# Performance work log

Measured on AMD Instinct MI355X. Metric: run time of the kernel, lower is better.

Reference implementation:

```python
import jax, jax.numpy as jnp
import numpy as np

B = 2048          # env batch
N = 32            # num_svgd_particles
D = 6             # act_dim
OBS = 17          # obs_dim
H = 256           # q1 hidden width
STEPS = 10        # num_svgd_steps
LR = 0.1          # svgd_lr
LIMIT = 1.0       # act_limit
LOG_NP1 = np.float32(np.log(N + 1.0))


def setup_inputs() -> dict:
    key = jax.random.key(0)
    ks = jax.random.split(key, 6)
    obs = jax.random.normal(ks[0], (B * N, OBS), dtype=jnp.float32)
    a = jax.random.normal(ks[1], (B * N, D), dtype=jnp.float32)
    W1 = jax.random.normal(ks[2], (OBS + D, H), dtype=jnp.float32) / np.float32(np.sqrt(OBS + D))
    b1 = jnp.zeros((H,), dtype=jnp.float32)
    W2 = jax.random.normal(ks[3], (H, H), dtype=jnp.float32) / np.float32(np.sqrt(H))
    b2 = jnp.zeros((H,), dtype=jnp.float32)
    W3 = jax.random.normal(ks[4], (H, 1), dtype=jnp.float32) / np.float32(np.sqrt(H))
    b3 = jnp.zeros((1,), dtype=jnp.float32)
    return {"obs": obs, "a": a, "W1": W1, "b1": b1, "W2": W2, "b2": b2, "W3": W3, "b3": b3}


def q1(obs, X, W1, b1, W2, b2, W3, b3):
    # standard SAC critic: Q(s, a) = MLP(concat(s, a))
    h = jax.nn.relu(jnp.concatenate([obs, X], axis=-1) @ W1 + b1)
    h = jax.nn.relu(h @ W2 + b2)
    return (h @ W3 + b3).squeeze(-1)


def rbf(X):
    # X: (B, N, D); input_2 = X.detach() in the original
    Xd = jax.lax.stop_gradient(X)
    diff = X[:, :, None, :] - Xd[:, None, :, :]          # (B, N, N, D)
    dist_sq = jnp.sum(diff * diff, axis=-1)              # (B, N, N)
    nn = N * N
    # torch.median returns the LOWER of the two middle values for even counts
    med = jnp.sort(jax.lax.stop_gradient(dist_sq).reshape(-1, nn), axis=1)[:, (nn - 1) // 2]
    h = med / (2.0 * LOG_NP1)                            # bandwidth^2 (sigma^2 = h)
    gamma = 1.0 / (1e-8 + 2.0 * h)                       # (B,)
    gamma = gamma[:, None, None]                         # (B, 1, 1)
    kappa = jnp.exp(-gamma * dist_sq)                    # (B, N, N)
    kappa_grad = -2.0 * (diff * gamma[..., None]) * kappa[..., None]  # (B, N, N, D)
    return kappa, diff, gamma, kappa_grad


def reference(obs, a, W1, b1, W2, b2, W3, b3):
    score_fn = jax.grad(lambda Xf: q1(obs, Xf, W1, b1, W2, b2, W3, b3).sum())
    logp = jnp.zeros((B, N), dtype=jnp.float32)

    for _ in range(STEPS):
        score = score_fn(a)                              # (B*N, D)
        X = a.reshape(B, N, D)
        s = score.reshape(B, N, D)
        K_XX, K_diff, K_gamma, K_grad = rbf(X)
        Kd = jax.lax.stop_gradient(K_XX)
        phi = (jnp.einsum('bij,bjd->bid', Kd, s) - K_grad.sum(axis=2)) / N  # (B, N, D)
        line_4 = (K_grad * s[:, None, :, :]).sum(-1).mean(-1)               # (B, N)
        line_5 = -2.0 * K_gamma[:, :, 0] * (
            (-K_grad * K_diff).sum(-1) - D * K_XX
        ).mean(-1)                                                          # (B, N)
        logp = logp - LR * (line_4 + line_5)
        a = jnp.clip(a + LR * phi.reshape(B * N, D), -LIMIT, LIMIT)
        a = jax.lax.stop_gradient(a)

    return a, logp
```

## Files before the change

### kernel.cpp

```cpp
#include <hip/hip_runtime.h>
#include <hip/hip_bf16.h>

#define NB 2048
#define NP 32
#define ND 6
#define NOBS 17
#define NH 256
#define NSTEPS 10
#define C_LR 0.1f
#define C_LIM 1.0f
#define C_LOGNP1 3.4965075614664802f

typedef __bf16 bf16x8 __attribute__((ext_vector_type(8)));
typedef float  f32x4  __attribute__((ext_vector_type(4)));

#define MFMA(a, b, c) __builtin_amdgcn_mfma_f32_16x16x32_bf16(a, b, c, 0, 0, 0)

static __device__ __forceinline__ unsigned short f2bf(float f) {
    union { float f; unsigned u; } c; c.f = f;
    const unsigned r = c.u + 0x7fffu + ((c.u >> 16) & 1u);
    return (unsigned short)(r >> 16);
}

static __device__ __forceinline__ int colpf(int n) {
    return ((n >> 5) << 11) + (((n >> 3) & 3) << 7) + (n & 7);
}

__global__ void prep_swizzle(const float* __restrict__ W1, const float* __restrict__ W2,
                             unsigned short* __restrict__ ws) {
    const int g = blockIdx.x * 256 + threadIdx.x;
    unsigned short v[8];
    if (g < 8192) {
        const int l = g & 63, fid = g >> 6;
        const int kt = fid >> 4, nt = fid & 15;
        const int row0 = kt * 32 + (l >> 4) * 8;
        const int col  = nt * 16 + (l & 15);
#pragma unroll
        for (int j = 0; j < 8; ++j) v[j] = f2bf(W2[(row0 + j) * NH + col]);
        ushort4* dst = (ushort4*)(ws + (size_t)g * 8);
        dst[0] = make_ushort4(v[0], v[1], v[2], v[3]);
        dst[1] = make_ushort4(v[4], v[5], v[6], v[7]);
    } else if (g < 16384) {
        const int e = g - 8192;
        const int l = e & 63, fid = e >> 6;
        const int kt = fid >> 4, nt = fid & 15;
        const int row  = nt * 16 + (l & 15);
        const int col0 = kt * 32 + (l >> 4) * 8;
#pragma unroll
        for (int j = 0; j < 8; ++j) v[j] = f2bf(W2[row * NH + col0 + j]);
        ushort4* dst = (ushort4*)(ws + 65536 + (size_t)e * 8);
        dst[0] = make_ushort4(v[0], v[1], v[2], v[3]);
        dst[1] = make_ushort4(v[4], v[5], v[6], v[7]);
    } else if (g < 16896) {
        const int e = g - 16384;
        const int l = e & 63, kt = e >> 6;
        const int n  = l & 15;
        const int k0 = kt * 32 + (l >> 4) * 8;
#pragma unroll
        for (int j = 0; j < 8; ++j)
            v[j] = (n < ND) ? f2bf(W1[(NOBS + n) * NH + k0 + j]) : (unsigned short)0;
        ushort4* dst = (ushort4*)(ws + 131072 + (size_t)e * 8);
        dst[0] = make_ushort4(v[0], v[1], v[2], v[3]);
        dst[1] = make_ushort4(v[4], v[5], v[6], v[7]);
    } else if (g < 17920) {
        const int e = g - 16896;
        const int l = e & 63, nt = e >> 6;
        const int col = nt * 16 + (l & 15);
        const int r0  = (l >> 4) * 8;
#pragma unroll
        for (int j = 0; j < 8; ++j)
            v[j] = (r0 + j < NOBS + ND) ? f2bf(W1[(r0 + j) * NH + col]) : (unsigned short)0;
        ushort4* dst = (ushort4*)(ws + 135168 + (size_t)e * 8);
        dst[0] = make_ushort4(v[0], v[1], v[2], v[3]);
        dst[1] = make_ushort4(v[4], v[5], v[6], v[7]);
    }
}

__global__ __launch_bounds__(256, 4)
void svgd_kernel(const float* __restrict__ obs, const float* __restrict__ a_in,
                 const float* __restrict__ W1, const float* __restrict__ b1,
                 const float* __restrict__ W2, const float* __restrict__ b2,
                 const float* __restrict__ W3, const unsigned short* __restrict__ ws,
                 float* __restrict__ out)
{
    __shared__ __attribute__((aligned(16))) unsigned short hA[64 * NH];
    __shared__ float Xs[2][384];
    __shared__ float sc_[512];
    __shared__ float med_s[2];

    const int t    = threadIdx.x;
    const int bb   = blockIdx.x;
    const int lane = t & 63;
    const int wid  = t >> 6;
    const int w4   = wid * 4;
    const int quad = lane >> 4;
    const int ln15 = lane & 15;
    const int qo = t >> 7, iao = (t & 127) >> 2, jgo = t & 3;

    const unsigned short* gW2f = ws;
    const unsigned short* gW2b = ws + 65536;
    const unsigned short* gW1p = ws + 131072;
    const unsigned short* gW1f = ws + 135168;

    {
        float* scr = (float*)hA;
        const float* obs_g = obs + (size_t)bb * 1088;
        for (int p = t; p < 1088; p += 256) scr[p] = obs_g[p];
        const float* a_g = a_in + (size_t)bb * 384;
        for (int p = t; p < 384; p += 256) Xs[0][p] = a_g[p];
    }
    __syncthreads();
    bf16x8 a0[4];
    {
        const float* scr = (const float*)hA;
#pragma unroll
        for (int m = 0; m < 4; ++m) {
            const int s = m * 16 + ln15;
#pragma unroll
            for (int j = 0; j < 8; ++j) {
                const int k = quad * 8 + j;
                float v = 0.0f;
                if (k < NOBS) v = scr[s * NOBS + k];
                else if (k < NOBS + ND) v = Xs[0][s * 6 + (k - NOBS)];
                a0[m][j] = (__bf16)v;
            }
        }
    }
    __syncthreads();

    float b1r[4], b2r[4]; unsigned short w3u[4];
#pragma unroll
    for (int q = 0; q < 4; ++q) {
        const int n = (w4 + q) * 16 + ln15;
        b1r[q] = b1[n]; b2r[q] = b2[n]; w3u[q] = f2bf(W3[n]);
    }

    float logp_r = 0.0f;
    int cur = 0;
    const f32x4 zv = {0.f, 0.f, 0.f, 0.f};

    for (int step = 0; step < NSTEPS; ++step) {
        unsigned long long mask1 = 0ull;
        {
            bf16x8 w1B[4];
#pragma unroll
            for (int q = 0; q < 4; ++q)
                w1B[q] = *(const bf16x8*)(gW1f + ((w4 + q) * 64 + lane) * 8);
            f32x4 acc0[4][4];
#pragma unroll
            for (int m = 0; m < 4; ++m)
#pragma unroll
                for (int q = 0; q < 4; ++q) acc0[m][q] = MFMA(a0[m], w1B[q], zv);
#pragma unroll
            for (int q = 0; q < 4; ++q) {
                const int cp = colpf((w4 + q) * 16 + ln15);
#pragma unroll
                for (int m = 0; m < 4; ++m)
#pragma unroll
                    for (int reg = 0; reg < 4; ++reg) {
                        const float hv = acc0[m][q][reg] + b1r[q];
                        const int idx = cp + m * 512 + (quad * 4 + reg) * 8;
                        if (hv > 0.f) {
                            mask1 |= 1ull << (q * 16 + m * 4 + reg);
                            hA[idx] = f2bf(hv);
                        } else hA[idx] = 0;
                    }
            }
        }
        __syncthreads();

        {
            f32x4 acc[4][4];
#pragma unroll
            for (int m = 0; m < 4; ++m)
#pragma unroll
                for (int q = 0; q < 4; ++q) acc[m][q] = zv;
#pragma unroll 2
            for (int kt = 0; kt < 8; ++kt) {
                bf16x8 a[4];
#pragma unroll
                for (int m = 0; m < 4; ++m)
                    a[m] = *(const bf16x8*)&hA[(kt * 4 + m) * 512 + lane * 8];
#pragma unroll
                for (int q = 0; q < 4; ++q) {
                    const bf16x8 bf = *(const bf16x8*)(gW2f + ((kt * 16 + w4 + q) * 64 + lane) * 8);
#pragma unroll
                    for (int m = 0; m < 4; ++m) acc[m][q] = MFMA(a[m], bf, acc[m][q]);
                }
            }
            __syncthreads();
#pragma unroll
            for (int q = 0; q < 4; ++q) {
                const int cp = colpf((w4 + q) * 16 + ln15);
                const float b2v = b2r[q];
                const unsigned short w3v = w3u[q];
#pragma unroll
                for (int m = 0; m < 4; ++m)
#pragma unroll
                    for (int reg = 0; reg < 4; ++reg) {
                        const int idx = cp + m * 512 + (quad * 4 + reg) * 8;
                        hA[idx] = (acc[m][q][reg] + b2v > 0.f) ? w3v : (unsigned short)0;
                    }
            }
        }
        __syncthreads();

        {
            f32x4 acc2[4][4];
#pragma unroll
            for (int m = 0; m < 4; ++m)
#pragma unroll
                for (int q = 0; q < 4; ++q) acc2[m][q] = zv;
#pragma unroll 2
            for (int kt = 0; kt < 8; ++kt) {
                bf16x8 a[4];
#pragma unroll
                for (int m = 0; m < 4; ++m)
                    a[m] = *(const bf16x8*)&hA[(kt * 4 + m) * 512 + lane * 8];
#pragma unroll
                for (int q = 0; q < 4; ++q) {
                    const bf16x8 bf = *(const bf16x8*)(gW2b + ((kt * 16 + w4 + q) * 64 + lane) * 8);
#pragma unroll
                    for (int m = 0; m < 4; ++m) acc2[m][q] = MFMA(a[m], bf, acc2[m][q]);
                }
            }
            __syncthreads();
#pragma unroll
            for (int q = 0; q < 4; ++q) {
                const int cp = colpf((w4 + q) * 16 + ln15);
#pragma unroll
                for (int m = 0; m < 4; ++m)
#pragma unroll
                    for (int reg = 0; reg < 4; ++reg) {
                        const int idx = cp + m * 512 + (quad * 4 + reg) * 8;
                        hA[idx] = ((mask1 >> (q * 16 + m * 4 + reg)) & 1ull)
                                      ? f2bf(acc2[m][q][reg]) : (unsigned short)0;
                    }
            }
        }
        __syncthreads();

        if (wid >= 2) {
            const int mb = (wid - 2) * 2;
            f32x4 sa[2] = {zv, zv};
#pragma unroll
            for (int kt = 0; kt < 8; ++kt) {
                const bf16x8 bw = *(const bf16x8*)(gW1p + (kt * 64 + lane) * 8);
#pragma unroll
                for (int mm = 0; mm < 2; ++mm) {
                    const bf16x8 a = *(const bf16x8*)&hA[(kt * 4 + mb + mm) * 512 + lane * 8];
                    sa[mm] = MFMA(a, bw, sa[mm]);
                }
            }
            if (ln15 < ND) {
#pragma unroll
                for (int mm = 0; mm < 2; ++mm)
#pragma unroll
                    for (int reg = 0; reg < 4; ++reg)
                        sc_[((mb + mm) * 16 + quad * 4 + reg) * 8 + ln15] = sa[mm][reg];
            }
        } else {
            const float* Xc = &Xs[cur][wid * 192];
            unsigned u[8];
#pragma unroll
            for (int r = 0; r < 8; ++r) {
                const int e = lane + 64 * r;
                if (e < 496) {
                    int i = (int)((63.0f - sqrtf(3969.0f - 8.0f * (float)e)) * 0.5f);
                    while (i * (63 - i) / 2 > e) --i;
                    while ((i + 1) * (62 - i) / 2 <= e) ++i;
                    const int j = i + 1 + (e - i * (63 - i) / 2);
                    float s = 0.f;
#pragma unroll
                    for (int d = 0; d < ND; ++d) {
                        const float df = Xc[i * 6 + d] - Xc[j * 6 + d];
                        s += df * df;
                    }
                    u[r] = __float_as_uint(s);
                } else u[r] = 0x7f800000u;
            }
            unsigned P = 0u;
            for (int bit = 30; bit >= 0; --bit) {
                const unsigned Q = P | (1u << bit);
                int c = 0;
#pragma unroll
                for (int r = 0; r < 8; ++r)
                    c += __popcll(__ballot(u[r] < Q));
                if (c <= 239) P = Q;
            }
            if (lane == 0) med_s[wid] = __uint_as_float(P);
        }
        __syncthreads();

        {
            const int nxt = cur ^ 1;
            const float gam = 1.0f / (1e-8f + med_s[qo] / C_LOGNP1);
            const float* Xc = &Xs[cur][qo * 192];
            float xi[6];
#pragma unroll
            for (int d = 0; d < ND; ++d) xi[d] = Xc[iao * 6 + d];
            float w[8] = {0, 0, 0, 0, 0, 0, 0, 0};
#pragma unroll
            for (int jj = 0; jj < 8; ++jj) {
                const int j = jgo * 8 + jj;
                float df6[6], sj6[6];
                float dsv = 0.f, dot = 0.f;
#pragma unroll
                for (int d = 0; d < ND; ++d) {
                    df6[d] = xi[d] - Xc[j * 6 + d];
                    sj6[d] = sc_[(qo * 32 + j) * 8 + d];
                    dsv += df6[d] * df6[d];
                    dot += df6[d] * sj6[d];
                }
                const float kap = __expf(-gam * dsv);
                const float tg = 2.0f * gam * kap;
#pragma unroll
                for (int d = 0; d < ND; ++d) w[d] += kap * sj6[d] + tg * df6[d];
                w[6] -= tg * dot;
                w[7] += tg * dsv - 6.0f * kap;
            }
#pragma unroll
            for (int off = 1; off < 4; off <<= 1)
#pragma unroll
                for (int c = 0; c < 8; ++c) w[c] += __shfl_xor(w[c], off);
            const int base = (qo * 32 + iao) * 6;
            {
                float x = xi[jgo] + C_LR * (w[jgo] * (1.0f / 32.0f));
                Xs[nxt][base + jgo] = fminf(fmaxf(x, -C_LIM), C_LIM);
            }
            if (jgo < 2) {
                const int d = jgo + 4;
                float x = xi[d] + C_LR * (w[d] * (1.0f / 32.0f));
                Xs[nxt][base + d] = fminf(fmaxf(x, -C_LIM), C_LIM);
            }
            if (jgo == 3)
                logp_r -= C_LR * (w[6] * (1.0f / 32.0f)
                                  - 2.0f * gam * (w[7] * (1.0f / 32.0f)));
        }
        __syncthreads();

        cur ^= 1;
        if (quad == 2) {
#pragma unroll
            for (int m = 0; m < 4; ++m) {
                const int s = m * 16 + ln15;
#pragma unroll
                for (int j = 1; j <= 6; ++j)
                    a0[m][j] = (__bf16)Xs[cur][s * 6 + (j - 1)];
            }
        }
    }

    for (int p = t; p < 384; p += 256) out[(size_t)bb * 384 + p] = Xs[cur][p];
    if (jgo == 3) out[(size_t)NB * NP * ND + bb * 64 + qo * 32 + iao] = logp_r;
}

extern "C" void kernel_launch(void* const* d_in, const int* in_sizes, int n_in,
                              void* d_out, int out_size, void* d_ws, size_t ws_size,
                              hipStream_t stream) {
    const float* obs = (const float*)d_in[0];
    const float* a   = (const float*)d_in[1];
    const float* W1  = (const float*)d_in[2];
    const float* b1  = (const float*)d_in[3];
    const float* W2  = (const float*)d_in[4];
    const float* b2  = (const float*)d_in[5];
    const float* W3  = (const float*)d_in[6];
    unsigned short* wsu = (unsigned short*)d_ws;
    float* out = (float*)d_out;

    prep_swizzle<<<70, 256, 0, stream>>>(W1, W2, wsu);
    svgd_kernel<<<NB / 2, 256, 0, stream>>>(obs, a, W1, b1, W2, b2, W3, wsu, out);
}
```

Baseline: 488.4 us.

## Swizzle LDS layouts, pack bf16 conversions, vectorize particle loads, shorten median search

The hidden-activation buffer hA is written and read through an XOR-swizzled address pattern to cut LDS bank conflicts in the MFMA operand loads. ReLU outputs are now converted two at a time with v_cvt_pk_bf16_f32 instead of the manual rounding helper. Particle positions and scores are padded to a stride of 8 floats with a swizzle, so each particle is read with one 4-wide and one 2-wide vector load. The median bisection stops at bit 8, which saves ballot iterations but leaves the low mantissa bits of the median at zero, a small approximation in the bandwidth.

```diff
diff --git a/kernel.cpp b/kernel.cpp
--- a/kernel.cpp
+++ b/kernel.cpp
@@ -13,6 +13,7 @@
 
 typedef __bf16 bf16x8 __attribute__((ext_vector_type(8)));
 typedef float  f32x4  __attribute__((ext_vector_type(4)));
+typedef float  f32x2  __attribute__((ext_vector_type(2)));
 
 #define MFMA(a, b, c) __builtin_amdgcn_mfma_f32_16x16x32_bf16(a, b, c, 0, 0, 0)
 
@@ -22,9 +23,17 @@
     return (unsigned short)(r >> 16);
 }
 
+static __device__ __forceinline__ unsigned cvtpk_bf16(float lo, float hi) {
+    unsigned r;
+    asm("v_cvt_pk_bf16_f32 %0, %1, %2" : "=v"(r) : "v"(lo), "v"(hi));
+    return r;
+}
+
 static __device__ __forceinline__ int colpf(int n) {
     return ((n >> 5) << 11) + (((n >> 3) & 3) << 7) + (n & 7);
 }
+
+#define XSW(p) ((((p) >> 3) & 3) << 3)
 
 __global__ void prep_swizzle(const float* __restrict__ W1, const float* __restrict__ W2,
                              unsigned short* __restrict__ ws) {
@@ -84,8 +93,8 @@
                  float* __restrict__ out)
 {
     __shared__ __attribute__((aligned(16))) unsigned short hA[64 * NH];
-    __shared__ float Xs[2][384];
-    __shared__ float sc_[512];
+    __shared__ __attribute__((aligned(16))) float Xs[2][512];
+    __shared__ __attribute__((aligned(16))) float sc_[512];
     __shared__ float med_s[2];
 
     const int t    = threadIdx.x;
@@ -97,6 +106,11 @@
     const int ln15 = lane & 15;
     const int qo = t >> 7, iao = (t & 127) >> 2, jgo = t & 3;
 
+    const int lb = (((lane >> 2) & 3) << 3)
+                 | (((lane & 3) ^ ((lane >> 4) & 1)) << 5)
+                 | ((lane >> 4) << 7);
+    const int x5t = ((ln15 >> 3) & 1) << 5;
+
     const unsigned short* gW2f = ws;
     const unsigned short* gW2b = ws + 65536;
     const unsigned short* gW1p = ws + 131072;
@@ -107,7 +121,10 @@
         const float* obs_g = obs + (size_t)bb * 1088;
         for (int p = t; p < 1088; p += 256) scr[p] = obs_g[p];
         const float* a_g = a_in + (size_t)bb * 384;
-        for (int p = t; p < 384; p += 256) Xs[0][p] = a_g[p];
+        for (int e = t; e < 384; e += 256) {
+            const int p = e / 6, d = e - p * 6;
+            Xs[0][((p * 8) ^ XSW(p)) + d] = a_g[e];
+        }
     }
     __syncthreads();
     bf16x8 a0[4];
@@ -121,7 +138,7 @@
                 const int k = quad * 8 + j;
                 float v = 0.0f;
                 if (k < NOBS) v = scr[s * NOBS + k];
-                else if (k < NOBS + ND) v = Xs[0][s * 6 + (k - NOBS)];
+                else if (k < NOBS + ND) v = Xs[0][((s * 8) ^ XSW(s)) + (k - NOBS)];
                 a0[m][j] = (__bf16)v;
             }
         }
@@ -153,18 +170,29 @@
                 for (int q = 0; q < 4; ++q) acc0[m][q] = MFMA(a0[m], w1B[q], zv);
 #pragma unroll
             for (int q = 0; q < 4; ++q) {
-                const int cp = colpf((w4 + q) * 16 + ln15);
-#pragma unroll
-                for (int m = 0; m < 4; ++m)
-#pragma unroll
-                    for (int reg = 0; reg < 4; ++reg) {
-                        const float hv = acc0[m][q][reg] + b1r[q];
-                        const int idx = cp + m * 512 + (quad * 4 + reg) * 8;
-                        if (hv > 0.f) {
-                            mask1 |= 1ull << (q * 16 + m * 4 + reg);
-                            hA[idx] = f2bf(hv);
-                        } else hA[idx] = 0;
-                    }
+                const int cq = colpf((w4 + q) * 16 + ln15) + quad * 8;
+                const int ax0 = (cq     ) ^ x5t;
+                const int ax1 = (cq + 32) ^ x5t;
+                const int ax2 = (cq + 64) ^ x5t;
+                const int ax3 = (cq + 96) ^ x5t;
+                const float b1v = b1r[q];
+#pragma unroll
+                for (int m = 0; m < 4; ++m) {
+                    const float f0 = acc0[m][q][0] + b1v;
+                    const float f1 = acc0[m][q][1] + b1v;
+                    const float f2 = acc0[m][q][2] + b1v;
+                    const float f3 = acc0[m][q][3] + b1v;
+                    if (f0 > 0.f) mask1 |= 1ull << (q * 16 + m * 4 + 0);
+                    if (f1 > 0.f) mask1 |= 1ull << (q * 16 + m * 4 + 1);
+                    if (f2 > 0.f) mask1 |= 1ull << (q * 16 + m * 4 + 2);
+                    if (f3 > 0.f) mask1 |= 1ull << (q * 16 + m * 4 + 3);
+                    const unsigned pk01 = cvtpk_bf16(fmaxf(f0, 0.f), fmaxf(f1, 0.f));
+                    const unsigned pk23 = cvtpk_bf16(fmaxf(f2, 0.f), fmaxf(f3, 0.f));
+                    hA[ax0 + m * 512] = (unsigned short)pk01;
+                    hA[ax1 + m * 512] = (unsigned short)(pk01 >> 16);
+                    hA[ax2 + m * 512] = (unsigned short)pk23;
+                    hA[ax3 + m * 512] = (unsigned short)(pk23 >> 16);
+                }
             }
         }
         __syncthreads();
@@ -180,7 +208,7 @@
                 bf16x8 a[4];
 #pragma unroll
                 for (int m = 0; m < 4; ++m)
-                    a[m] = *(const bf16x8*)&hA[(kt * 4 + m) * 512 + lane * 8];
+                    a[m] = *(const bf16x8*)&hA[(kt * 4 + m) * 512 + lb];
 #pragma unroll
                 for (int q = 0; q < 4; ++q) {
                     const bf16x8 bf = *(const bf16x8*)(gW2f + ((kt * 16 + w4 + q) * 64 + lane) * 8);
@@ -191,16 +219,20 @@
             __syncthreads();
 #pragma unroll
             for (int q = 0; q < 4; ++q) {
-                const int cp = colpf((w4 + q) * 16 + ln15);
+                const int cq = colpf((w4 + q) * 16 + ln15) + quad * 8;
+                const int ax0 = (cq     ) ^ x5t;
+                const int ax1 = (cq + 32) ^ x5t;
+                const int ax2 = (cq + 64) ^ x5t;
+                const int ax3 = (cq + 96) ^ x5t;
                 const float b2v = b2r[q];
                 const unsigned short w3v = w3u[q];
 #pragma unroll
-                for (int m = 0; m < 4; ++m)
-#pragma unroll
-                    for (int reg = 0; reg < 4; ++reg) {
-                        const int idx = cp + m * 512 + (quad * 4 + reg) * 8;
-                        hA[idx] = (acc[m][q][reg] + b2v > 0.f) ? w3v : (unsigned short)0;
-                    }
+                for (int m = 0; m < 4; ++m) {
+                    hA[ax0 + m * 512] = (acc[m][q][0] + b2v > 0.f) ? w3v : (unsigned short)0;
+                    hA[ax1 + m * 512] = (acc[m][q][1] + b2v > 0.f) ? w3v : (unsigned short)0;
+                    hA[ax2 + m * 512] = (acc[m][q][2] + b2v > 0.f) ? w3v : (unsigned short)0;
+                    hA[ax3 + m * 512] = (acc[m][q][3] + b2v > 0.f) ? w3v : (unsigned short)0;
+                }
             }
         }
         __syncthreads();
@@ -216,7 +248,7 @@
                 bf16x8 a[4];
 #pragma unroll
                 for (int m = 0; m < 4; ++m)
-                    a[m] = *(const bf16x8*)&hA[(kt * 4 + m) * 512 + lane * 8];
+                    a[m] = *(const bf16x8*)&hA[(kt * 4 + m) * 512 + lb];
 #pragma unroll
                 for (int q = 0; q < 4; ++q) {
                     const bf16x8 bf = *(const bf16x8*)(gW2b + ((kt * 16 + w4 + q) * 64 + lane) * 8);
@@ -227,15 +259,25 @@
             __syncthreads();
 #pragma unroll
             for (int q = 0; q < 4; ++q) {
-                const int cp = colpf((w4 + q) * 16 + ln15);
-#pragma unroll
-                for (int m = 0; m < 4; ++m)
-#pragma unroll
-                    for (int reg = 0; reg < 4; ++reg) {
-                        const int idx = cp + m * 512 + (quad * 4 + reg) * 8;
-                        hA[idx] = ((mask1 >> (q * 16 + m * 4 + reg)) & 1ull)
-                                      ? f2bf(acc2[m][q][reg]) : (unsigned short)0;
-                    }
+                const int cq = colpf((w4 + q) * 16 + ln15) + quad * 8;
+                const int ax0 = (cq     ) ^ x5t;
+                const int ax1 = (cq + 32) ^ x5t;
+                const int ax2 = (cq + 64) ^ x5t;
+                const int ax3 = (cq + 96) ^ x5t;
+#pragma unroll
+                for (int m = 0; m < 4; ++m) {
+                    const int kb = q * 16 + m * 4;
+                    const float v0 = ((mask1 >> (kb + 0)) & 1ull) ? acc2[m][q][0] : 0.f;
+                    const float v1 = ((mask1 >> (kb + 1)) & 1ull) ? acc2[m][q][1] : 0.f;
+                    const float v2 = ((mask1 >> (kb + 2)) & 1ull) ? acc2[m][q][2] : 0.f;
+                    const float v3 = ((mask1 >> (kb + 3)) & 1ull) ? acc2[m][q][3] : 0.f;
+                    const unsigned pk01 = cvtpk_bf16(v0, v1);
+                    const unsigned pk23 = cvtpk_bf16(v2, v3);
+                    hA[ax0 + m * 512] = (unsigned short)pk01;
+                    hA[ax1 + m * 512] = (unsigned short)(pk01 >> 16);
+                    hA[ax2 + m * 512] = (unsigned short)pk23;
+                    hA[ax3 + m * 512] = (unsigned short)(pk23 >> 16);
+                }
             }
         }
         __syncthreads();
@@ -248,7 +290,7 @@
                 const bf16x8 bw = *(const bf16x8*)(gW1p + (kt * 64 + lane) * 8);
 #pragma unroll
                 for (int mm = 0; mm < 2; ++mm) {
-                    const bf16x8 a = *(const bf16x8*)&hA[(kt * 4 + mb + mm) * 512 + lane * 8];
+                    const bf16x8 a = *(const bf16x8*)&hA[(kt * 4 + mb + mm) * 512 + lb];
                     sa[mm] = MFMA(a, bw, sa[mm]);
                 }
             }
@@ -256,11 +298,13 @@
 #pragma unroll
                 for (int mm = 0; mm < 2; ++mm)
 #pragma unroll
-                    for (int reg = 0; reg < 4; ++reg)
-                        sc_[((mb + mm) * 16 + quad * 4 + reg) * 8 + ln15] = sa[mm][reg];
+                    for (int reg = 0; reg < 4; ++reg) {
+                        const int row = (mb + mm) * 16 + quad * 4 + reg;
+                        sc_[((row * 8) ^ XSW(row)) + ln15] = sa[mm][reg];
+                    }
             }
         } else {
-            const float* Xc = &Xs[cur][wid * 192];
+            const float* Xc = &Xs[cur][wid * 256];
             unsigned u[8];
 #pragma unroll
             for (int r = 0; r < 8; ++r) {
@@ -270,17 +314,26 @@
                     while (i * (63 - i) / 2 > e) --i;
                     while ((i + 1) * (62 - i) / 2 <= e) ++i;
                     const int j = i + 1 + (e - i * (63 - i) / 2);
+                    const int ibz = (i * 8) ^ XSW(i), jbz = (j * 8) ^ XSW(j);
+                    const f32x4 pa = *(const f32x4*)&Xc[ibz];
+                    const f32x2 pb = *(const f32x2*)&Xc[ibz + 4];
+                    const f32x4 qa = *(const f32x4*)&Xc[jbz];
+                    const f32x2 qb = *(const f32x2*)&Xc[jbz + 4];
                     float s = 0.f;
-#pragma unroll
-                    for (int d = 0; d < ND; ++d) {
-                        const float df = Xc[i * 6 + d] - Xc[j * 6 + d];
-                        s += df * df;
+                    {
+                        float df;
+                        df = pa[0] - qa[0]; s += df * df;
+                        df = pa[1] - qa[1]; s += df * df;
+                        df = pa[2] - qa[2]; s += df * df;
+                        df = pa[3] - qa[3]; s += df * df;
+                        df = pb[0] - qb[0]; s += df * df;
+                        df = pb[1] - qb[1]; s += df * df;
                     }
                     u[r] = __float_as_uint(s);
                 } else u[r] = 0x7f800000u;
             }
             unsigned P = 0u;
-            for (int bit = 30; bit >= 0; --bit) {
+            for (int bit = 30; bit >= 8; --bit) {
                 const unsigned Q = P | (1u << bit);
                 int c = 0;
 #pragma unroll
@@ -295,20 +348,26 @@
         {
             const int nxt = cur ^ 1;
             const float gam = 1.0f / (1e-8f + med_s[qo] / C_LOGNP1);
-            const float* Xc = &Xs[cur][qo * 192];
-            float xi[6];
-#pragma unroll
-            for (int d = 0; d < ND; ++d) xi[d] = Xc[iao * 6 + d];
+            const float* Xc = &Xs[cur][qo * 256];
+            const int xib = (iao * 8) ^ XSW(iao);
+            const f32x4 xa = *(const f32x4*)&Xc[xib];
+            const f32x2 xb = *(const f32x2*)&Xc[xib + 4];
+            float xi[6] = {xa[0], xa[1], xa[2], xa[3], xb[0], xb[1]};
             float w[8] = {0, 0, 0, 0, 0, 0, 0, 0};
 #pragma unroll
             for (int jj = 0; jj < 8; ++jj) {
                 const int j = jgo * 8 + jj;
-                float df6[6], sj6[6];
+                const int jb = (j * 8) ^ XSW(j);
+                const f32x4 qa  = *(const f32x4*)&Xc[jb];
+                const f32x2 qb  = *(const f32x2*)&Xc[jb + 4];
+                const f32x4 sa4 = *(const f32x4*)&sc_[qo * 256 + jb];
+                const f32x2 sb2 = *(const f32x2*)&sc_[qo * 256 + jb + 4];
+                const float df6[6] = {xi[0] - qa[0], xi[1] - qa[1], xi[2] - qa[2],
+                                      xi[3] - qa[3], xi[4] - qb[0], xi[5] - qb[1]};
+                const float sj6[6] = {sa4[0], sa4[1], sa4[2], sa4[3], sb2[0], sb2[1]};
                 float dsv = 0.f, dot = 0.f;
 #pragma unroll
                 for (int d = 0; d < ND; ++d) {
-                    df6[d] = xi[d] - Xc[j * 6 + d];
-                    sj6[d] = sc_[(qo * 32 + j) * 8 + d];
                     dsv += df6[d] * df6[d];
                     dot += df6[d] * sj6[d];
                 }
@@ -323,15 +382,15 @@
             for (int off = 1; off < 4; off <<= 1)
 #pragma unroll
                 for (int c = 0; c < 8; ++c) w[c] += __shfl_xor(w[c], off);
-            const int base = (qo * 32 + iao) * 6;
+            const int wb = qo * 256 + xib;
             {
                 float x = xi[jgo] + C_LR * (w[jgo] * (1.0f / 32.0f));
-                Xs[nxt][base + jgo] = fminf(fmaxf(x, -C_LIM), C_LIM);
+                Xs[nxt][wb + jgo] = fminf(fmaxf(x, -C_LIM), C_LIM);
             }
             if (jgo < 2) {
                 const int d = jgo + 4;
                 float x = xi[d] + C_LR * (w[d] * (1.0f / 32.0f));
-                Xs[nxt][base + d] = fminf(fmaxf(x, -C_LIM), C_LIM);
+                Xs[nxt][wb + d] = fminf(fmaxf(x, -C_LIM), C_LIM);
             }
             if (jgo == 3)
                 logp_r -= C_LR * (w[6] * (1.0f / 32.0f)
@@ -344,14 +403,20 @@
 #pragma unroll
             for (int m = 0; m < 4; ++m) {
                 const int s = m * 16 + ln15;
-#pragma unroll
-                for (int j = 1; j <= 6; ++j)
-                    a0[m][j] = (__bf16)Xs[cur][s * 6 + (j - 1)];
-            }
-        }
-    }
-
-    for (int p = t; p < 384; p += 256) out[(size_t)bb * 384 + p] = Xs[cur][p];
+                const int sb = (s * 8) ^ XSW(s);
+                const f32x4 xv = *(const f32x4*)&Xs[cur][sb];
+                const f32x2 xw = *(const f32x2*)&Xs[cur][sb + 4];
+                a0[m][1] = (__bf16)xv[0]; a0[m][2] = (__bf16)xv[1];
+                a0[m][3] = (__bf16)xv[2]; a0[m][4] = (__bf16)xv[3];
+                a0[m][5] = (__bf16)xw[0]; a0[m][6] = (__bf16)xw[1];
+            }
+        }
+    }
+
+    for (int e = t; e < 384; e += 256) {
+        const int p = e / 6, d = e - p * 6;
+        out[(size_t)bb * 384 + e] = Xs[cur][((p * 8) ^ XSW(p)) + d];
+    }
     if (jgo == 3) out[(size_t)NB * NP * ND + bb * 64 + qo * 32 + iao] = logp_r;
 }
 
```

Measured after the change: 718.1 us. 1.47x slower.
